# Performance work log

Hardware: AMD Instinct MI355X
Metric: run time of the kernel (lower is better)

The kernel has to match this reference:

```python
import jax, jax.numpy as jnp
import numpy as np

RESID = 1024
HEADS = 16
HEAD_DIM = 64


def setup_inputs() -> dict:
    key = jax.random.key(0)
    ks = jax.random.split(key, 6)
    B, S = 2, 2048
    residual_stream = jax.random.normal(ks[0], (B, S, RESID), dtype=jnp.float32)
    # per-head qkv linear params, stacked over heads: [H, resid, 3*head_dim]
    W_qkv = jax.random.normal(ks[1], (HEADS, RESID, 3 * HEAD_DIM), dtype=jnp.float32) * (1.0 / np.sqrt(RESID))
    b_qkv = jax.random.normal(ks[2], (HEADS, 3 * HEAD_DIM), dtype=jnp.float32) * 0.01
    # output projection resid -> resid
    W_o = jax.random.normal(ks[3], (RESID, RESID), dtype=jnp.float32) * (1.0 / np.sqrt(RESID))
    b_o = jax.random.normal(ks[4], (RESID,), dtype=jnp.float32) * 0.01
    return {"residual_stream": residual_stream, "W_qkv": W_qkv, "b_qkv": b_qkv, "W_o": W_o, "b_o": b_o}


def reference(residual_stream, W_qkv, b_qkv, W_o, b_o):
    # qkv per head: [B, H, S, 3*D]
    qkv = jnp.einsum('bsr,hrd->bhsd', residual_stream, W_qkv) + b_qkv[None, :, None, :]
    q = qkv[..., :HEAD_DIM]
    k = qkv[..., HEAD_DIM:2 * HEAD_DIM]
    v = qkv[..., 2 * HEAD_DIM:]
    # NOTE: original has no causal mask; softmax over full key axis
    scores = jnp.einsum('bhsd,bhtd->bhst', q, k) / jnp.sqrt(jnp.float32(HEAD_DIM))
    attn = jax.nn.softmax(scores, axis=-1)
    out = jnp.einsum('bhst,bhtd->bhsd', attn, v)  # [B, H, S, D]
    B, H, S, D = out.shape
    out = out.transpose(0, 2, 1, 3).reshape(B, S, H * D)  # concat heads -> [B, S, resid]
    return out @ W_o + b_o
```

## Files before the change

kernel.cpp:

```cpp
#include <hip/hip_runtime.h>
#include <hip/hip_bf16.h>

#define B_ 2
#define S_ 2048
#define H_ 16
#define HD 64
#define R_ 1024
#define N_ (B_*S_)

typedef unsigned short ushort_t;
typedef short bf16x8 __attribute__((ext_vector_type(8)));
typedef float f32x4 __attribute__((ext_vector_type(4)));
typedef float f32x16 __attribute__((ext_vector_type(16)));

#define MFMA(a,b,c) __builtin_amdgcn_mfma_f32_16x16x32_bf16(a,b,c,0,0,0)
#define MFMA32(a,b,c) __builtin_amdgcn_mfma_f32_32x32x16_bf16(a,b,c,0,0,0)
#define GLD16(g,l) __builtin_amdgcn_global_load_lds( \
    (const __attribute__((address_space(1))) void*)(g), \
    (__attribute__((address_space(3))) void*)(l), 16, 0, 0)

__device__ __forceinline__ unsigned short f2bf(float f) {
  unsigned int u = __builtin_bit_cast(unsigned int, f);
  u += 0x7fffu + ((u >> 16) & 1u);
  return (unsigned short)(u >> 16);
}

__device__ __forceinline__ unsigned int cvtpk(float lo, float hi) {
  unsigned int r;
  asm("v_cvt_pk_bf16_f32 %0, %1, %2" : "=v"(r) : "v"(lo), "v"(hi));
  return r;
}

__device__ __forceinline__ void plswap(unsigned int &a, unsigned int &b) {
  asm volatile("v_permlane32_swap_b32 %0, %1" : "+v"(a), "+v"(b));
}

__device__ __forceinline__ bf16x8 ld8(const ushort_t* p) {
  return *(const bf16x8*)p;
}

__global__ __launch_bounds__(256) void k_convert_x(const float* __restrict__ x,
                                                   ushort_t* __restrict__ xb) {
  int i = blockIdx.x * 256 + threadIdx.x;
  float4 v = ((const float4*)x)[i];
  ushort4 o;
  o.x = f2bf(v.x); o.y = f2bf(v.y); o.z = f2bf(v.z); o.w = f2bf(v.w);
  ((ushort4*)xb)[i] = o;
}

__global__ __launch_bounds__(256) void k_transpose(const float* __restrict__ in,
                                                   ushort_t* __restrict__ out,
                                                   int rows, int cols) {
  __shared__ float t[64][65];
  const size_t bo = (size_t)blockIdx.z * rows * cols;
  const int r0 = blockIdx.x * 64, c0 = blockIdx.y * 64;
  const int tx = threadIdx.x & 63, ty = threadIdx.x >> 6;
  #pragma unroll
  for (int i = 0; i < 16; i++) {
    int r = ty * 16 + i;
    t[r][tx] = in[bo + (size_t)(r0 + r) * cols + c0 + tx];
  }
  __syncthreads();
  #pragma unroll
  for (int i = 0; i < 16; i++) {
    int c = ty * 16 + i;
    out[bo + (size_t)(c0 + c) * rows + r0 + tx] = f2bf(t[tx][c]);
  }
}

__global__ __launch_bounds__(256, 2) void k_qkv(
    const ushort_t* __restrict__ Xb, const ushort_t* __restrict__ WT,
    const float* __restrict__ bqkv,
    ushort_t* __restrict__ Q, ushort_t* __restrict__ K, ushort_t* __restrict__ Vt) {
  __shared__ ushort_t lA[2][128 * 32];
  __shared__ ushort_t lB[2][192 * 32];
  const int m0 = blockIdx.x * 128;
  const int h  = blockIdx.y;
  const int tid = threadIdx.x;
  const int w = tid >> 6, l = tid & 63;
  const int lr = l & 15, lg = l >> 4;
  const int wr = w >> 1, wc = w & 1;

  const ushort_t* Asrc = Xb + (size_t)m0 * R_;
  const ushort_t* Bsrc = WT + (size_t)h * 192 * R_;
  const int arow = l >> 2;
  const int acol = (l & 3) * 8;

  f32x4 acc[4][6];
  const f32x4 fz = {0.f, 0.f, 0.f, 0.f};
  #pragma unroll
  for (int m = 0; m < 4; m++)
    #pragma unroll
    for (int n = 0; n < 6; n++) acc[m][n] = fz;

  auto stage = [&](int buf, int kt) {
    const int k0 = kt * 32;
    #pragma unroll
    for (int i = 0; i < 2; i++) {
      int chunk = w + 4 * i;
      GLD16(Asrc + (size_t)(chunk * 16 + arow) * R_ + k0 + acol, &lA[buf][chunk * 512]);
    }
    #pragma unroll
    for (int i = 0; i < 3; i++) {
      int chunk = w + 4 * i;
      GLD16(Bsrc + (size_t)(chunk * 16 + arow) * R_ + k0 + acol, &lB[buf][chunk * 512]);
    }
  };

  stage(0, 0);
  asm volatile("s_waitcnt vmcnt(0)" ::: "memory");
  __syncthreads();

  int cur = 0;
  for (int kt = 0; kt < 32; ++kt) {
    if (kt < 31) stage(cur ^ 1, kt + 1);
    bf16x8 af[4], bfr[6];
    #pragma unroll
    for (int m = 0; m < 4; m++)
      af[m] = ld8(&lA[cur][(wr * 64 + m * 16 + lr) * 32 + lg * 8]);
    #pragma unroll
    for (int n = 0; n < 6; n++)
      bfr[n] = ld8(&lB[cur][(wc * 96 + n * 16 + lr) * 32 + lg * 8]);
    __builtin_amdgcn_s_setprio(1);
    #pragma unroll
    for (int m = 0; m < 4; m++)
      #pragma unroll
      for (int n = 0; n < 6; n++)
        acc[m][n] = MFMA(af[m], bfr[n], acc[m][n]);
    __builtin_amdgcn_s_setprio(0);
    asm volatile("s_waitcnt vmcnt(0)" ::: "memory");
    __syncthreads();
    cur ^= 1;
  }

  #pragma unroll
  for (int n = 0; n < 6; n++) {
    const int col = wc * 96 + n * 16 + lr;
    const float bias = bqkv[h * 192 + col];
    #pragma unroll
    for (int m = 0; m < 4; m++) {
      const int rb = m0 + wr * 64 + m * 16 + lg * 4;
      #pragma unroll
      for (int r = 0; r < 4; r++) {
        float v = acc[m][n][r] + bias;
        int srow = rb + r;
        int b = srow >> 11, s = srow & 2047;
        size_t bh = (size_t)b * H_ + h;
        if (col < 64) {
          Q[(bh * S_ + s) * HD + col] = f2bf(v * 0.1803368801111137f);
        } else if (col < 128) {
          int d = col - 64;
          K[(bh * S_ + s) * HD + d] = f2bf(v);
        } else {
          int d = col - 128;
          Vt[(bh * HD + d) * S_ + s] = f2bf(v);
        }
      }
    }
  }
}

__global__ __launch_bounds__(256, 2) void k_attn(
    const ushort_t* __restrict__ Q, const ushort_t* __restrict__ K,
    const ushort_t* __restrict__ Vt, ushort_t* __restrict__ AO) {
  __shared__ ushort_t lK[2][64 * 64];
  __shared__ ushort_t lV[2][64 * 64];
  const int qt = blockIdx.x;
  const int bh = blockIdx.y;
  const int b = bh >> 4, h = bh & 15;
  const int tid = threadIdx.x, w = tid >> 6, l = tid & 63;
  const int lq = l & 31, hi = l >> 5;

  const ushort_t* Qb = Q + (size_t)bh * S_ * HD;
  const ushort_t* Kb = K + (size_t)bh * S_ * HD;
  const ushort_t* Vb = Vt + (size_t)bh * HD * S_;

  bf16x8 qf[4];
  {
    int qrow = qt * 128 + 32 * w + lq;
    #pragma unroll
    for (int kd = 0; kd < 4; kd++)
      qf[kd] = ld8(&Qb[(size_t)qrow * HD + kd * 16 + hi * 8]);
  }

  const int sr = l >> 3;
  const int scol = l & 7;
  bf16x8 kreg[2], vreg[2];
  auto issue = [&](int t0) {
    #pragma unroll
    for (int i = 0; i < 2; i++) {
      int r = (w * 2 + i) * 8 + sr;
      kreg[i] = ld8(&Kb[(size_t)(t0 + r) * HD + scol * 8]);
      vreg[i] = ld8(&Vb[(size_t)r * S_ + t0 + scol * 8]);
    }
  };
  auto commit = [&](int buf) {
    #pragma unroll
    for (int i = 0; i < 2; i++) {
      int r = (w * 2 + i) * 8 + sr;
      int off = r * 64 + ((scol ^ (r & 7)) * 8);
      *(bf16x8*)&lK[buf][off] = kreg[i];
      *(bf16x8*)&lV[buf][off] = vreg[i];
    }
  };

  const f32x16 fz16 = {0};
  const bf16x8 onesv = {0x3F80, 0x3F80, 0x3F80, 0x3F80, 0x3F80, 0x3F80, 0x3F80, 0x3F80};
  f32x16 oacc[2];
  f32x16 ssv;
  oacc[0] = fz16; oacc[1] = fz16; ssv = fz16;

  const int xr = lq & 7;

  issue(0);
  commit(0);
  __syncthreads();

  int cur = 0;
  for (int kt = 0; kt < 32; ++kt) {
    if (kt < 31) issue((kt + 1) * 64);

    f32x16 sc0 = fz16, sc1 = fz16;
    __builtin_amdgcn_s_setprio(1);
    #pragma unroll
    for (int kd = 0; kd < 4; kd++) {
      bf16x8 ka0 = ld8(&lK[cur][lq * 64 + (((kd * 2 + hi) ^ xr) * 8)]);
      bf16x8 ka1 = ld8(&lK[cur][(32 + lq) * 64 + (((kd * 2 + hi) ^ xr) * 8)]);
      sc0 = MFMA32(ka0, qf[kd], sc0);
      sc1 = MFMA32(ka1, qf[kd], sc1);
    }
    __builtin_amdgcn_s_setprio(0);

    #pragma unroll
    for (int n = 0; n < 2; n++) {
      const f32x16 scv = n ? sc1 : sc0;
      float e[16];
      #pragma unroll
      for (int r = 0; r < 16; r++) e[r] = exp2f(scv[r]);
      #pragma unroll
      for (int sl = 0; sl < 2; sl++) {
        unsigned int X  = cvtpk(e[8 * sl + 0], e[8 * sl + 1]);
        unsigned int Y  = cvtpk(e[8 * sl + 2], e[8 * sl + 3]);
        unsigned int X2 = cvtpk(e[8 * sl + 4], e[8 * sl + 5]);
        unsigned int Y2 = cvtpk(e[8 * sl + 6], e[8 * sl + 7]);
        plswap(X, X2);
        plswap(Y, Y2);
        int4 wv = {(int)X, (int)Y, (int)X2, (int)Y2};
        bf16x8 pa = __builtin_bit_cast(bf16x8, wv);
        const int ks = n * 2 + sl;
        __builtin_amdgcn_s_setprio(1);
        ssv = MFMA32(pa, onesv, ssv);
        #pragma unroll
        for (int db = 0; db < 2; db++) {
          bf16x8 vb = ld8(&lV[cur][(db * 32 + lq) * 64 + (((ks * 2 + hi) ^ xr) * 8)]);
          oacc[db] = MFMA32(pa, vb, oacc[db]);
        }
        __builtin_amdgcn_s_setprio(0);
      }
    }

    if (kt < 31) commit(cur ^ 1);
    __syncthreads();
    cur ^= 1;
  }

  float inv[16];
  #pragma unroll
  for (int reg = 0; reg < 16; reg++) inv[reg] = 1.0f / ssv[reg];
  #pragma unroll
  for (int db = 0; db < 2; db++)
    #pragma unroll
    for (int reg = 0; reg < 16; reg++) {
      int qloc = (reg & 3) + 8 * (reg >> 2) + 4 * hi;
      int s = qt * 128 + 32 * w + qloc;
      float o = oacc[db][reg] * inv[reg];
      AO[(size_t)(b * S_ + s) * R_ + h * HD + db * 32 + lq] = f2bf(o);
    }
}

__global__ __launch_bounds__(256, 2) void k_out(
    const ushort_t* __restrict__ AO, const ushort_t* __restrict__ WoT,
    const float* __restrict__ bo, float* __restrict__ out) {
  __shared__ ushort_t lA[2][128 * 32];
  __shared__ ushort_t lB[2][128 * 32];
  const int m0 = blockIdx.x * 128, n0 = blockIdx.y * 128;
  const int tid = threadIdx.x, w = tid >> 6, l = tid & 63;
  const int lr = l & 15, lg = l >> 4;
  const int wr = w >> 1, wc = w & 1;
  const ushort_t* Asrc = AO + (size_t)m0 * R_;
  const ushort_t* Bsrc = WoT + (size_t)n0 * R_;
  const int arow = l >> 2, acol = (l & 3) * 8;

  f32x4 acc[4][4];
  const f32x4 fz = {0.f, 0.f, 0.f, 0.f};
  #pragma unroll
  for (int m = 0; m < 4; m++)
    #pragma unroll
    for (int n = 0; n < 4; n++) acc[m][n] = fz;

  auto stage = [&](int buf, int kt) {
    const int k0 = kt * 32;
    #pragma unroll
    for (int i = 0; i < 2; i++) {
      int chunk = w + 4 * i;
      GLD16(Asrc + (size_t)(chunk * 16 + arow) * R_ + k0 + acol, &lA[buf][chunk * 512]);
      GLD16(Bsrc + (size_t)(chunk * 16 + arow) * R_ + k0 + acol, &lB[buf][chunk * 512]);
    }
  };

  stage(0, 0);
  asm volatile("s_waitcnt vmcnt(0)" ::: "memory");
  __syncthreads();

  int cur = 0;
  for (int kt = 0; kt < 32; ++kt) {
    if (kt < 31) stage(cur ^ 1, kt + 1);
    bf16x8 af[4], bfr[4];
    #pragma unroll
    for (int m = 0; m < 4; m++)
      af[m] = ld8(&lA[cur][(wr * 64 + m * 16 + lr) * 32 + lg * 8]);
    #pragma unroll
    for (int n = 0; n < 4; n++)
      bfr[n] = ld8(&lB[cur][(wc * 64 + n * 16 + lr) * 32 + lg * 8]);
    __builtin_amdgcn_s_setprio(1);
    #pragma unroll
    for (int m = 0; m < 4; m++)
      #pragma unroll
      for (int n = 0; n < 4; n++)
        acc[m][n] = MFMA(af[m], bfr[n], acc[m][n]);
    __builtin_amdgcn_s_setprio(0);
    asm volatile("s_waitcnt vmcnt(0)" ::: "memory");
    __syncthreads();
    cur ^= 1;
  }

  #pragma unroll
  for (int n = 0; n < 4; n++) {
    const int col = n0 + wc * 64 + n * 16 + lr;
    const float bias = bo[col];
    #pragma unroll
    for (int m = 0; m < 4; m++) {
      const int row = m0 + wr * 64 + m * 16 + lg * 4;
      #pragma unroll
      for (int r = 0; r < 4; r++)
        out[(size_t)(row + r) * R_ + col] = acc[m][n][r] + bias;
    }
  }
}

extern "C" void kernel_launch(void* const* d_in, const int* in_sizes, int n_in,
                              void* d_out, int out_size, void* d_ws, size_t ws_size,
                              hipStream_t stream) {
  const float* resid = (const float*)d_in[0];
  const float* Wqkv  = (const float*)d_in[1];
  const float* bqkv  = (const float*)d_in[2];
  const float* Wo    = (const float*)d_in[3];
  const float* bo    = (const float*)d_in[4];
  float* out = (float*)d_out;

  ushort_t* Xb  = (ushort_t*)d_ws;
  ushort_t* WT  = Xb  + (size_t)N_ * R_;
  ushort_t* WoT = WT  + (size_t)H_ * 192 * R_;
  ushort_t* Qd  = WoT + (size_t)R_ * R_;
  ushort_t* Kd  = Qd  + (size_t)B_ * H_ * S_ * HD;
  ushort_t* Vtd = Kd  + (size_t)B_ * H_ * S_ * HD;
  ushort_t* AOd = Vtd + (size_t)B_ * H_ * S_ * HD;

  k_convert_x<<<dim3(4096), dim3(256), 0, stream>>>(resid, Xb);
  k_transpose<<<dim3(16, 3, 16), dim3(256), 0, stream>>>(Wqkv, WT, 1024, 192);
  k_transpose<<<dim3(16, 16, 1), dim3(256), 0, stream>>>(Wo, WoT, 1024, 1024);
  k_qkv<<<dim3(32, 16), dim3(256), 0, stream>>>(Xb, WT, bqkv, Qd, Kd, Vtd);
  k_attn<<<dim3(16, 32), dim3(256), 0, stream>>>(Qd, Kd, Vtd, AOd);
  k_out<<<dim3(32, 8), dim3(256), 0, stream>>>(AOd, WoT, bo, out);
}
```

Before: 135.0 us.

## Merge prep kernels and software-pipeline attention with triple-buffered K/V

Folds the bf16 conversion and both weight transposes into one prep launch, which removes two kernel launches. The attention kernel moves to a three-buffer LDS ring, so the QK^T MFMAs for the next tile run while softmax and PV run for the current one. It also uses hardware exp2 and rcp intrinsics and precomputed load pointers. This adds LDS use and register pressure from holding two sets of scores, which could hurt occupancy at two blocks per CU.

After: 120.2 us (median of 2 runs). -11.0%, faster.

```diff
diff --git a/kernel.cpp b/kernel.cpp
--- a/kernel.cpp
+++ b/kernel.cpp
@@ -35,36 +35,63 @@
   asm volatile("v_permlane32_swap_b32 %0, %1" : "+v"(a), "+v"(b));
 }
 
+#if __has_builtin(__builtin_amdgcn_exp2f)
+__device__ __forceinline__ float EXP2(float x) { return __builtin_amdgcn_exp2f(x); }
+#else
+__device__ __forceinline__ float EXP2(float x) {
+  float r; asm("v_exp_f32 %0, %1" : "=v"(r) : "v"(x)); return r;
+}
+#endif
+
+#if __has_builtin(__builtin_amdgcn_rcpf)
+__device__ __forceinline__ float RCP(float x) { return __builtin_amdgcn_rcpf(x); }
+#else
+__device__ __forceinline__ float RCP(float x) { return 1.0f / x; }
+#endif
+
 __device__ __forceinline__ bf16x8 ld8(const ushort_t* p) {
   return *(const bf16x8*)p;
 }
 
-__global__ __launch_bounds__(256) void k_convert_x(const float* __restrict__ x,
-                                                   ushort_t* __restrict__ xb) {
-  int i = blockIdx.x * 256 + threadIdx.x;
-  float4 v = ((const float4*)x)[i];
-  ushort4 o;
-  o.x = f2bf(v.x); o.y = f2bf(v.y); o.z = f2bf(v.z); o.w = f2bf(v.w);
-  ((ushort4*)xb)[i] = o;
-}
-
-__global__ __launch_bounds__(256) void k_transpose(const float* __restrict__ in,
-                                                   ushort_t* __restrict__ out,
-                                                   int rows, int cols) {
-  __shared__ float t[64][65];
-  const size_t bo = (size_t)blockIdx.z * rows * cols;
-  const int r0 = blockIdx.x * 64, c0 = blockIdx.y * 64;
-  const int tx = threadIdx.x & 63, ty = threadIdx.x >> 6;
+__device__ __forceinline__ void transpose_tile(const float* __restrict__ in,
+                                               ushort_t* __restrict__ out,
+                                               int rows, int cols, int rt, int ct,
+                                               float (*t)[65], int tid) {
+  const int r0 = rt * 64, c0 = ct * 64;
+  const int tx = tid & 63, ty = tid >> 6;
   #pragma unroll
   for (int i = 0; i < 16; i++) {
     int r = ty * 16 + i;
-    t[r][tx] = in[bo + (size_t)(r0 + r) * cols + c0 + tx];
+    t[r][tx] = in[(size_t)(r0 + r) * cols + c0 + tx];
   }
   __syncthreads();
   #pragma unroll
   for (int i = 0; i < 16; i++) {
     int c = ty * 16 + i;
-    out[bo + (size_t)(c0 + c) * rows + r0 + tx] = f2bf(t[tx][c]);
+    out[(size_t)(c0 + c) * rows + r0 + tx] = f2bf(t[tx][c]);
+  }
+}
+
+__global__ __launch_bounds__(256) void k_prep(
+    const float* __restrict__ x, ushort_t* __restrict__ xb,
+    const float* __restrict__ Wqkv, ushort_t* __restrict__ WT,
+    const float* __restrict__ Wo, ushort_t* __restrict__ WoT) {
+  __shared__ float t[64][65];
+  const int bid = blockIdx.x, tid = threadIdx.x;
+  if (bid < 4096) {
+    int i = bid * 256 + tid;
+    float4 v = ((const float4*)x)[i];
+    ushort4 o;
+    o.x = f2bf(v.x); o.y = f2bf(v.y); o.z = f2bf(v.z); o.w = f2bf(v.w);
+    ((ushort4*)xb)[i] = o;
+  } else if (bid < 4096 + 768) {
+    int tt = bid - 4096;
+    int z = tt / 48, rem = tt % 48;
+    transpose_tile(Wqkv + (size_t)z * 1024 * 192, WT + (size_t)z * 192 * 1024,
+                   1024, 192, rem % 16, rem / 16, t, tid);
+  } else {
+    int tt = bid - (4096 + 768);
+    transpose_tile(Wo, WoT, 1024, 1024, tt % 16, tt / 16, t, tid);
   }
 }
 
@@ -163,8 +190,8 @@
 __global__ __launch_bounds__(256, 2) void k_attn(
     const ushort_t* __restrict__ Q, const ushort_t* __restrict__ K,
     const ushort_t* __restrict__ Vt, ushort_t* __restrict__ AO) {
-  __shared__ ushort_t lK[2][64 * 64];
-  __shared__ ushort_t lV[2][64 * 64];
+  __shared__ ushort_t sK[3][64 * 64];
+  __shared__ ushort_t sV[3][64 * 64];
   const int qt = blockIdx.x;
   const int bh = blockIdx.y;
   const int b = bh >> 4, h = bh & 15;
@@ -185,97 +212,118 @@
 
   const int sr = l >> 3;
   const int scol = l & 7;
-  bf16x8 kreg[2], vreg[2];
-  auto issue = [&](int t0) {
-    #pragma unroll
-    for (int i = 0; i < 2; i++) {
-      int r = (w * 2 + i) * 8 + sr;
-      kreg[i] = ld8(&Kb[(size_t)(t0 + r) * HD + scol * 8]);
-      vreg[i] = ld8(&Vb[(size_t)r * S_ + t0 + scol * 8]);
-    }
-  };
-  auto commit = [&](int buf) {
-    #pragma unroll
-    for (int i = 0; i < 2; i++) {
-      int r = (w * 2 + i) * 8 + sr;
-      int off = r * 64 + ((scol ^ (r & 7)) * 8);
-      *(bf16x8*)&lK[buf][off] = kreg[i];
-      *(bf16x8*)&lV[buf][off] = vreg[i];
-    }
+  const int r0l = w * 16 + sr;
+  const ushort_t* kp = Kb + (size_t)r0l * HD + scol * 8;
+  const ushort_t* vp = Vb + (size_t)r0l * S_ + scol * 8;
+  bf16x8 kreg0, kreg1, vreg0, vreg1;
+  int tnext = 0;
+  auto issue = [&]() {
+    if (tnext < 32) {
+      kreg0 = ld8(kp); kreg1 = ld8(kp + 8 * HD);
+      vreg0 = ld8(vp); vreg1 = ld8(vp + 8 * S_);
+      kp += 64 * HD; vp += 64;
+    }
+    ++tnext;
+  };
+  const int coff0 = r0l * 64 + ((scol ^ sr) * 8);
+  const int coff1 = coff0 + 8 * 64;
+  auto commit = [&](ushort_t* bK, ushort_t* bV) {
+    *(bf16x8*)&bK[coff0] = kreg0; *(bf16x8*)&bK[coff1] = kreg1;
+    *(bf16x8*)&bV[coff0] = vreg0; *(bf16x8*)&bV[coff1] = vreg1;
   };
 
   const f32x16 fz16 = {0};
   const bf16x8 onesv = {0x3F80, 0x3F80, 0x3F80, 0x3F80, 0x3F80, 0x3F80, 0x3F80, 0x3F80};
-  f32x16 oacc[2];
-  f32x16 ssv;
-  oacc[0] = fz16; oacc[1] = fz16; ssv = fz16;
-
-  const int xr = lq & 7;
-
-  issue(0);
-  commit(0);
-  __syncthreads();
-
-  int cur = 0;
-  for (int kt = 0; kt < 32; ++kt) {
-    if (kt < 31) issue((kt + 1) * 64);
-
-    f32x16 sc0 = fz16, sc1 = fz16;
+  f32x16 oacc0 = fz16, oacc1 = fz16, ssv = fz16;
+
+  const int c = hi ^ (lq & 7);
+
+  auto QK = [&](const ushort_t* bK, f32x16& s0, f32x16& s1) {
+    f32x16 a0 = fz16, a1 = fz16;
     __builtin_amdgcn_s_setprio(1);
     #pragma unroll
     for (int kd = 0; kd < 4; kd++) {
-      bf16x8 ka0 = ld8(&lK[cur][lq * 64 + (((kd * 2 + hi) ^ xr) * 8)]);
-      bf16x8 ka1 = ld8(&lK[cur][(32 + lq) * 64 + (((kd * 2 + hi) ^ xr) * 8)]);
-      sc0 = MFMA32(ka0, qf[kd], sc0);
-      sc1 = MFMA32(ka1, qf[kd], sc1);
+      const int sl = ((kd * 2) ^ c) * 8;
+      bf16x8 ka0 = ld8(&bK[lq * 64 + sl]);
+      bf16x8 ka1 = ld8(&bK[(32 + lq) * 64 + sl]);
+      a0 = MFMA32(ka0, qf[kd], a0);
+      a1 = MFMA32(ka1, qf[kd], a1);
     }
     __builtin_amdgcn_s_setprio(0);
-
+    s0 = a0; s1 = a1;
+  };
+
+  auto SMPV = [&](const ushort_t* bV, f32x16 s0, f32x16 s1) {
     #pragma unroll
     for (int n = 0; n < 2; n++) {
-      const f32x16 scv = n ? sc1 : sc0;
+      const f32x16 scv = n ? s1 : s0;
       float e[16];
       #pragma unroll
-      for (int r = 0; r < 16; r++) e[r] = exp2f(scv[r]);
-      #pragma unroll
-      for (int sl = 0; sl < 2; sl++) {
-        unsigned int X  = cvtpk(e[8 * sl + 0], e[8 * sl + 1]);
-        unsigned int Y  = cvtpk(e[8 * sl + 2], e[8 * sl + 3]);
-        unsigned int X2 = cvtpk(e[8 * sl + 4], e[8 * sl + 5]);
-        unsigned int Y2 = cvtpk(e[8 * sl + 6], e[8 * sl + 7]);
+      for (int r = 0; r < 16; r++) e[r] = EXP2(scv[r]);
+      #pragma unroll
+      for (int sl2 = 0; sl2 < 2; sl2++) {
+        unsigned int X  = cvtpk(e[8 * sl2 + 0], e[8 * sl2 + 1]);
+        unsigned int Y  = cvtpk(e[8 * sl2 + 2], e[8 * sl2 + 3]);
+        unsigned int X2 = cvtpk(e[8 * sl2 + 4], e[8 * sl2 + 5]);
+        unsigned int Y2 = cvtpk(e[8 * sl2 + 6], e[8 * sl2 + 7]);
         plswap(X, X2);
         plswap(Y, Y2);
         int4 wv = {(int)X, (int)Y, (int)X2, (int)Y2};
         bf16x8 pa = __builtin_bit_cast(bf16x8, wv);
-        const int ks = n * 2 + sl;
+        const int ks = n * 2 + sl2;
+        const int sl3 = ((ks * 2) ^ c) * 8;
         __builtin_amdgcn_s_setprio(1);
         ssv = MFMA32(pa, onesv, ssv);
-        #pragma unroll
-        for (int db = 0; db < 2; db++) {
-          bf16x8 vb = ld8(&lV[cur][(db * 32 + lq) * 64 + (((ks * 2 + hi) ^ xr) * 8)]);
-          oacc[db] = MFMA32(pa, vb, oacc[db]);
+        {
+          bf16x8 vb0 = ld8(&bV[lq * 64 + sl3]);
+          bf16x8 vb1 = ld8(&bV[(32 + lq) * 64 + sl3]);
+          oacc0 = MFMA32(pa, vb0, oacc0);
+          oacc1 = MFMA32(pa, vb1, oacc1);
         }
         __builtin_amdgcn_s_setprio(0);
       }
     }
-
-    if (kt < 31) commit(cur ^ 1);
+  };
+
+  f32x16 scA0, scA1, scB0, scB1;
+  issue();
+  commit(sK[0], sV[0]);
+  issue();
+  __syncthreads();
+  QK(sK[0], scA0, scA1);
+  commit(sK[1], sV[1]);
+  __syncthreads();
+  issue();
+
+#define ABODY(C, N, O, SI0, SI1, SO0, SO1) \
+    QK(sK[N], SO0, SO1); \
+    SMPV(sV[C], SI0, SI1); \
+    commit(sK[O], sV[O]); \
+    issue(); \
     __syncthreads();
-    cur ^= 1;
-  }
-
-  float inv[16];
-  #pragma unroll
-  for (int reg = 0; reg < 16; reg++) inv[reg] = 1.0f / ssv[reg];
-  #pragma unroll
-  for (int db = 0; db < 2; db++)
-    #pragma unroll
-    for (int reg = 0; reg < 16; reg++) {
-      int qloc = (reg & 3) + 8 * (reg >> 2) + 4 * hi;
-      int s = qt * 128 + 32 * w + qloc;
-      float o = oacc[db][reg] * inv[reg];
-      AO[(size_t)(b * S_ + s) * R_ + h * HD + db * 32 + lq] = f2bf(o);
-    }
+
+  for (int kt = 0; kt < 30; kt += 6) {
+    ABODY(0, 1, 2, scA0, scA1, scB0, scB1)
+    ABODY(1, 2, 0, scB0, scB1, scA0, scA1)
+    ABODY(2, 0, 1, scA0, scA1, scB0, scB1)
+    ABODY(0, 1, 2, scB0, scB1, scA0, scA1)
+    ABODY(1, 2, 0, scA0, scA1, scB0, scB1)
+    ABODY(2, 0, 1, scB0, scB1, scA0, scA1)
+  }
+#undef ABODY
+
+  QK(sK[1], scB0, scB1);
+  SMPV(sV[0], scA0, scA1);
+  SMPV(sV[1], scB0, scB1);
+
+  #pragma unroll
+  for (int reg = 0; reg < 16; reg++) {
+    float inv = RCP(ssv[reg]);
+    int qloc = (reg & 3) + 8 * (reg >> 2) + 4 * hi;
+    int s = qt * 128 + 32 * w + qloc;
+    AO[(size_t)(b * S_ + s) * R_ + h * HD + lq] = f2bf(oacc0[reg] * inv);
+    AO[(size_t)(b * S_ + s) * R_ + h * HD + 32 + lq] = f2bf(oacc1[reg] * inv);
+  }
 }
 
 __global__ __launch_bounds__(256, 2) void k_out(
@@ -366,9 +414,7 @@
   ushort_t* Vtd = Kd  + (size_t)B_ * H_ * S_ * HD;
   ushort_t* AOd = Vtd + (size_t)B_ * H_ * S_ * HD;
 
-  k_convert_x<<<dim3(4096), dim3(256), 0, stream>>>(resid, Xb);
-  k_transpose<<<dim3(16, 3, 16), dim3(256), 0, stream>>>(Wqkv, WT, 1024, 192);
-  k_transpose<<<dim3(16, 16, 1), dim3(256), 0, stream>>>(Wo, WoT, 1024, 1024);
+  k_prep<<<dim3(4096 + 768 + 256), dim3(256), 0, stream>>>(resid, Xb, Wqkv, WT, Wo, WoT);
   k_qkv<<<dim3(32, 16), dim3(256), 0, stream>>>(Xb, WT, bqkv, Qd, Kd, Vtd);
   k_attn<<<dim3(16, 32), dim3(256), 0, stream>>>(Qd, Kd, Vtd, AOd);
   k_out<<<dim3(32, 8), dim3(256), 0, stream>>>(AOd, WoT, bo, out);
```
